# Kernel tuning notes

Measured on AMD Instinct MI355X. Metric: run time of the kernel, lower is better.

The kernel has to match this reference:

```python
import jax, jax.numpy as jnp
import numpy as np
from jax import lax

B, T, C, L = 4096, 256, 96, 16  # batch, timesteps, classes (blank=C-1), max label len
NEG = -1e30  # log-domain -inf surrogate (fp32-safe)


def setup_inputs() -> dict:
    key = jax.random.key(0)
    k1, k2 = jax.random.split(key)
    # ctc_batch_cost expects softmax probabilities over classes
    y_pred = jax.nn.softmax(jax.random.normal(k1, (B, T, C), jnp.float32), axis=-1)
    labels = jax.random.randint(k2, (B, L), 0, C - 1, dtype=jnp.int32)  # values < blank
    input_length = jnp.full((B, 1), T, dtype=jnp.int32)
    label_length = jnp.full((B, 1), L, dtype=jnp.int32)
    return {"y_pred": y_pred, "labels": labels,
            "input_length": input_length, "label_length": label_length}


def _ctc_batch_cost(y_pred, labels, input_length, label_length):
    # keras: log(y_pred + epsilon), then tf.nn.ctc_loss (which log-softmax-normalizes)
    eps = 1e-7  # keras backend epsilon
    logp = jax.nn.log_softmax(jnp.log(y_pred + eps), axis=-1)  # [B,T,C]
    Bn, Tn, Cn = y_pred.shape
    blank = Cn - 1  # keras CTC uses last class as blank
    Ln = labels.shape[1]
    S = 2 * Ln + 1  # extended state lattice: blank,l1,blank,...,lL,blank
    il = input_length[:, 0]
    ll = label_length[:, 0]

    # extended label sequence [B,S]: even states=blank, odd states=labels
    ext = jnp.full((Bn, S), blank, dtype=labels.dtype).at[:, 1::2].set(labels)
    s_idx = jnp.arange(S)
    state_valid = s_idx[None, :] < (2 * ll[:, None] + 1)  # [B,S]
    # skip transition s-2 -> s allowed only for label states with ext[s] != ext[s-2]
    diff = jnp.concatenate([jnp.zeros((Bn, 2), bool), ext[:, 2:] != ext[:, :-2]], axis=1)
    skip_ok = (s_idx[None, :] % 2 == 1) & diff  # [B,S]

    # emission log-probs per lattice state: emit[b,t,s] = logp[b,t,ext[b,s]] -> [T,B,S]
    emit = logp[jnp.arange(Bn)[:, None, None], jnp.arange(Tn)[None, :, None], ext[:, None, :]]
    emit = jnp.transpose(emit, (1, 0, 2))

    alpha0 = jnp.full((Bn, S), NEG, jnp.float32)
    alpha0 = alpha0.at[:, 0].set(emit[0, :, 0])
    alpha0 = alpha0.at[:, 1].set(jnp.where(ll >= 1, emit[0, :, 1], NEG))

    def step(alpha, xs):
        emit_t, t = xs
        p1 = jnp.pad(alpha[:, :-1], ((0, 0), (1, 0)), constant_values=NEG)
        p2 = jnp.pad(alpha[:, :-2], ((0, 0), (2, 0)), constant_values=NEG)
        p2 = jnp.where(skip_ok, p2, NEG)
        new = jnp.logaddexp(jnp.logaddexp(alpha, p1), p2) + emit_t
        new = jnpp_where = jnp.where(state_valid, new, NEG)
        alpha = jnp.where((t < il)[:, None], new, alpha)
        return alpha, None

    ts = jnp.arange(1, Tn)
    alpha_T, _ = lax.scan(step, alpha0, (emit[1:], ts))

    b_idx = jnp.arange(Bn)
    a_last_blank = alpha_T[b_idx, 2 * ll]
    a_last_label = alpha_T[b_idx, jnp.maximum(2 * ll - 1, 0)]
    log_p = jnp.where(ll > 0, jnp.logaddexp(a_last_blank, a_last_label), a_last_blank)
    return -log_p[:, None]  # [B,1], matching ctc_batch_cost


def reference(y_pred, labels, input_length, label_length):
    # CTCLossLayer computes ctc_batch_cost(labels, y_pred, input_length, label_length)
    # via add_loss; the loss is the op of interest, so we return it.
    return _ctc_batch_cost(y_pred, labels, input_length, label_length)
```

## Files before the change

kernel.cpp:

```cpp
#include <hip/hip_runtime.h>
#include <hip/hip_bf16.h>


__device__ __forceinline__ float dpp_shr1(float x) {
    int r = __builtin_amdgcn_update_dpp(0, __builtin_bit_cast(int, x),
                                        0x138 , 0xF, 0xF, true);
    return __builtin_bit_cast(float, r);
}

__global__ __launch_bounds__(256) void ctc_loss_kernel(
    const float* __restrict__ y_pred,
    const int*   __restrict__ labels,
    const int*   __restrict__ input_length,
    const int*   __restrict__ label_length,
    float*       __restrict__ out,
    int Bn)
{
    constexpr int T = 256, C = 96, L = 16;
    constexpr int blank = C - 1;
    constexpr float EPS = 1e-7f;

    const int lane = threadIdx.x & 63;
    const int b = blockIdx.x * 4 + (threadIdx.x >> 6);
    if (b >= Bn) return;

    const int il = input_length[b];
    const int ll = label_length[b];
    const int s  = lane;

    int  extc = blank;
    bool skip_ok = false;
    if (s < 33 && (s & 1)) {
        extc = labels[b * L + (s >> 1)];
        if (s >= 3) skip_ok = (extc != labels[b * L + (s >> 1) - 1]);
    }
    const bool valid = (s < 2 * ll + 1);

    const float* colp = y_pred + (size_t)b * T * C + extc;

    float z0 = colp[0];
    float z1 = colp[C];
    float z2 = colp[2 * C];
    float z3 = colp[3 * C];

    float a = 0.0f, logC = 0.0f;

    auto step = [&](float yv, int t) {
        float p1 = dpp_shr1(a);
        float p2 = dpp_shr1(p1);
        p2 = skip_ok ? p2 : 0.0f;
        float nw = (a + p1 + p2) * yv;
        a = (t < il) ? nw : a;
    };

#define DPPMAX(mv, ctrl)                                                      \
    do { int s_ = __builtin_amdgcn_update_dpp(0, __builtin_bit_cast(int, mv), \
                                              (ctrl), 0xF, 0xF, true);        \
         mv = fmaxf(mv, __builtin_bit_cast(float, s_)); } while (0)

    auto rescale = [&]() {
        a = valid ? a : 0.0f;
        float m = a;
        DPPMAX(m, 0x111);
        DPPMAX(m, 0x112);
        DPPMAX(m, 0x114);
        DPPMAX(m, 0x118);
        DPPMAX(m, 0x142);
        DPPMAX(m, 0x143);
        m = __builtin_bit_cast(float,
                __builtin_amdgcn_readlane(__builtin_bit_cast(int, m), 63));
        logC += __logf(m);
        a *= __builtin_amdgcn_rcpf(m);
    };

    a = ((s == 0) | ((s == 1) & (ll >= 1))) ? z0 : 0.0f;

    {
        const float* bp = colp + (size_t)4 * C;
        float n0 = bp[0], n1 = bp[C], n2 = bp[2 * C], n3 = bp[3 * C];
        step(z1, 1); step(z2, 2); step(z3, 3);
        rescale();
        z0 = n0; z1 = n1; z2 = n2; z3 = n3;
    }
    for (int jb = 1; jb < 64; ++jb) {
        float n0 = 0.0f, n1 = 0.0f, n2 = 0.0f, n3 = 0.0f;
        if (jb < 63) {
            const float* bp = colp + (size_t)(4 * (jb + 1)) * C;
            n0 = bp[0]; n1 = bp[C]; n2 = bp[2 * C]; n3 = bp[3 * C];
        }
        const int tb = 4 * jb;
        step(z0, tb); step(z1, tb + 1); step(z2, tb + 2); step(z3, tb + 3);
        rescale();
        z0 = n0; z1 = n1; z2 = n2; z3 = n3;
    }

    const int i_b = 2 * ll;
    const int i_l = (2 * ll - 1 > 0) ? (2 * ll - 1) : 0;
    const float ab = __shfl(a, i_b, 64);
    const float al = __shfl(a, i_l, 64);
    const float p  = (ll > 0) ? (ab + al) : ab;
    const float loss = (float)il * logf(1.0f + (float)C * EPS) - logC - __logf(p);
    if (lane == 0) out[b] = loss;
#undef DPPMAX
}

extern "C" void kernel_launch(void* const* d_in, const int* in_sizes, int n_in,
                              void* d_out, int out_size, void* d_ws, size_t ws_size,
                              hipStream_t stream) {
    const float* y_pred       = (const float*)d_in[0];
    const int*   labels       = (const int*)d_in[1];
    const int*   input_length = (const int*)d_in[2];
    const int*   label_length = (const int*)d_in[3];
    float*       out          = (float*)d_out;

    const int B = in_sizes[2];
    const int blocks = (B + 3) / 4;
    ctc_loss_kernel<<<blocks, 256, 0, stream>>>(y_pred, labels, input_length,
                                                label_length, out, B);
}
```

Measured before the change: 72.21 us.

## Stage y_pred rows into LDS via async global_load_lds with triple buffering

Instead of each lane gathering its own strided column element from global memory, every wave now copies whole 8-timestep chunks of y_pred (768 floats) into LDS with coalesced 16-byte global_load_lds transfers. A three-slot ring buffer with explicit vmcnt waits keeps loads in flight while the DPP recurrence runs, and the rescale is done once per 8 steps instead of once per 4. The aim is to turn scattered uncoalesced gathers into full-line coalesced loads and hide memory latency. It adds LDS usage and hand-counted waitcnt ordering. There is no LDS read barrier, so it depends on each wave consuming only its own region, and the longer rescale interval carries a small risk of underflow.

```diff
diff --git a/kernel.cpp b/kernel.cpp
--- a/kernel.cpp
+++ b/kernel.cpp
@@ -7,6 +7,10 @@
                                         0x138 , 0xF, 0xF, true);
     return __builtin_bit_cast(float, r);
 }
+
+#define AS1(p) ((const __attribute__((address_space(1))) void*)(p))
+#define AS3(p) ((__attribute__((address_space(3))) void*)(p))
+#define VMW(n) asm volatile("s_waitcnt vmcnt(" #n ")" ::: "memory")
 
 __global__ __launch_bounds__(256) void ctc_loss_kernel(
     const float* __restrict__ y_pred,
@@ -20,8 +24,11 @@
     constexpr int blank = C - 1;
     constexpr float EPS = 1e-7f;
 
+    __shared__ float smem[4][3][768];
+
     const int lane = threadIdx.x & 63;
-    const int b = blockIdx.x * 4 + (threadIdx.x >> 6);
+    const int wv   = threadIdx.x >> 6;
+    const int b = blockIdx.x * 4 + wv;
     if (b >= Bn) return;
 
     const int il = input_length[b];
@@ -36,14 +43,17 @@
     }
     const bool valid = (s < 2 * ll + 1);
 
-    const float* colp = y_pred + (size_t)b * T * C + extc;
-
-    float z0 = colp[0];
-    float z1 = colp[C];
-    float z2 = colp[2 * C];
-    float z3 = colp[3 * C];
+    const float* gbase = y_pred + (size_t)b * T * C;
 
     float a = 0.0f, logC = 0.0f;
+
+    auto stage = [&](int grp, int slot) {
+        const float* gp = gbase + (size_t)grp * 768 + lane * 4;
+        float* lp = &smem[wv][slot][0];
+        __builtin_amdgcn_global_load_lds(AS1(gp),       AS3(lp),       16, 0, 0);
+        __builtin_amdgcn_global_load_lds(AS1(gp + 256), AS3(lp + 256), 16, 0, 0);
+        __builtin_amdgcn_global_load_lds(AS1(gp + 512), AS3(lp + 512), 16, 0, 0);
+    };
 
     auto step = [&](float yv, int t) {
         float p1 = dpp_shr1(a);
@@ -61,38 +71,40 @@
     auto rescale = [&]() {
         a = valid ? a : 0.0f;
         float m = a;
-        DPPMAX(m, 0x111);
-        DPPMAX(m, 0x112);
-        DPPMAX(m, 0x114);
-        DPPMAX(m, 0x118);
-        DPPMAX(m, 0x142);
-        DPPMAX(m, 0x143);
+        DPPMAX(m, 0x111); DPPMAX(m, 0x112); DPPMAX(m, 0x114); DPPMAX(m, 0x118);
+        DPPMAX(m, 0x142); DPPMAX(m, 0x143);
         m = __builtin_bit_cast(float,
                 __builtin_amdgcn_readlane(__builtin_bit_cast(int, m), 63));
         logC += __logf(m);
         a *= __builtin_amdgcn_rcpf(m);
     };
 
-    a = ((s == 0) | ((s == 1) & (ll >= 1))) ? z0 : 0.0f;
+    auto proc8 = [&](int t0, int slot, bool first) {
+        float z[8];
+        #pragma unroll
+        for (int r = 0; r < 8; ++r)
+            z[r] = smem[wv][slot][r * 96 + extc];
+        if (first) a = ((s == 0) | ((s == 1) & (ll >= 1))) ? z[0] : 0.0f;
+        else       step(z[0], t0);
+        step(z[1], t0 + 1); step(z[2], t0 + 2); step(z[3], t0 + 3);
+        step(z[4], t0 + 4); step(z[5], t0 + 5); step(z[6], t0 + 6);
+        step(z[7], t0 + 7);
+        rescale();
+    };
 
-    {
-        const float* bp = colp + (size_t)4 * C;
-        float n0 = bp[0], n1 = bp[C], n2 = bp[2 * C], n3 = bp[3 * C];
-        step(z1, 1); step(z2, 2); step(z3, 3);
-        rescale();
-        z0 = n0; z1 = n1; z2 = n2; z3 = n3;
+    stage(0, 0); stage(1, 1); stage(2, 2);
+
+    VMW(6); proc8(0,  0, true );  stage(3, 0);
+    VMW(6); proc8(8,  1, false);  stage(4, 1);
+    VMW(6); proc8(16, 2, false);  stage(5, 2);
+
+    for (int g = 3; g <= 27; g += 3) {
+        VMW(6); proc8(8 * g,       0, false);  stage(g + 3, 0);
+        VMW(6); proc8(8 * (g + 1), 1, false);  stage(g + 4, 1);
+        VMW(6); proc8(8 * (g + 2), 2, false);  if (g != 27) stage(g + 5, 2);
     }
-    for (int jb = 1; jb < 64; ++jb) {
-        float n0 = 0.0f, n1 = 0.0f, n2 = 0.0f, n3 = 0.0f;
-        if (jb < 63) {
-            const float* bp = colp + (size_t)(4 * (jb + 1)) * C;
-            n0 = bp[0]; n1 = bp[C]; n2 = bp[2 * C]; n3 = bp[3 * C];
-        }
-        const int tb = 4 * jb;
-        step(z0, tb); step(z1, tb + 1); step(z2, tb + 2); step(z3, tb + 3);
-        rescale();
-        z0 = n0; z1 = n1; z2 = n2; z3 = n3;
-    }
+    VMW(3); proc8(240, 0, false);
+    VMW(0); proc8(248, 1, false);
 
     const int i_b = 2 * ll;
     const int i_l = (2 * ll - 1 > 0) ? (2 * ll - 1) : 0;
```

After: 74.08 us. +2.6%, slower.
